# Kernel tuning notes

Hardware: AMD Instinct MI355X
Metric: run time of the kernel (lower is better)

Reference implementation:

```python
import jax, jax.numpy as jnp
import numpy as np

B, T, OBS, ENC, H, A = 32, 512, 256, 1024, 1024, 64
AR_COEF, TAR_COEF = 0.01, 0.01
LN_EPS = 1e-5


def setup_inputs() -> dict:
    key = jax.random.key(0)
    ks = jax.random.split(key, 8)
    s = 0.02  # weight scale to keep activations in a sane range
    # PyTorch LSTM bias init in source: zeros, forget-gate slice [H:2H] = 1.0 (both b_ih and b_hh)
    b_gate = jnp.zeros((4 * H,), jnp.float32).at[H:2 * H].set(1.0)
    return {
        "obs": jax.random.normal(ks[0], (B, T, OBS), jnp.float32),
        "hxs": jnp.zeros((B, H), jnp.float32),
        "cxs": jnp.zeros((B, H), jnp.float32),
        "W1": jax.random.normal(ks[1], (ENC, OBS), jnp.float32) * s,
        "b1": jnp.zeros((ENC,), jnp.float32),
        "W2": jax.random.normal(ks[2], (ENC, ENC), jnp.float32) * s,
        "b2": jnp.zeros((ENC,), jnp.float32),
        "W_ih": jax.random.normal(ks[3], (4 * H, ENC), jnp.float32) * s,
        "W_hh": jax.random.normal(ks[4], (4 * H, H), jnp.float32) * s,
        "b_ih": b_gate,
        "b_hh": b_gate,
        "ln_g": jnp.ones((H,), jnp.float32),
        "ln_b": jnp.zeros((H,), jnp.float32),
        "Wa": jax.random.normal(ks[5], (A, H), jnp.float32) * s,
        "ba": jnp.zeros((A,), jnp.float32),
        "Wc": jax.random.normal(ks[6], (1, H), jnp.float32) * s,
        "bc": jnp.zeros((1,), jnp.float32),
    }


def reference(obs, hxs, cxs, W1, b1, W2, b2, W_ih, W_hh, b_ih, b_hh,
              ln_g, ln_b, Wa, ba, Wc, bc):
    # Encoder: Linear -> SiLU -> Linear -> SiLU
    enc = jax.nn.silu(obs @ W1.T + b1)
    enc = jax.nn.silu(enc @ W2.T + b2)  # (B,T,ENC)

    # LSTM (WeightDrop is identity in eval mode / p=0). Precompute input gates.
    gx = enc @ W_ih.T + (b_ih + b_hh)  # (B,T,4H)

    def step(carry, g_t):
        h, c = carry
        g = g_t + h @ W_hh.T  # (B,4H), PyTorch gate order: i, f, g, o
        i, f, gc, o = jnp.split(g, 4, axis=-1)
        c = jax.nn.sigmoid(f) * c + jax.nn.sigmoid(i) * jnp.tanh(gc)
        h = jax.nn.sigmoid(o) * jnp.tanh(c)
        return (h, c), h

    (h_n, c_n), hs = jax.lax.scan(step, (hxs, cxs), jnp.swapaxes(gx, 0, 1))
    out = jnp.swapaxes(hs, 0, 1)  # (B,T,H)

    # LayerNorm
    mu = out.mean(-1, keepdims=True)
    var = out.var(-1, keepdims=True)
    out = (out - mu) / jnp.sqrt(var + LN_EPS) * ln_g + ln_b

    ar_loss = jnp.mean(out ** 2) * AR_COEF
    tar_loss = jnp.mean((out[:, 1:, :] - out[:, :-1, :]) ** 2) * TAR_COEF

    logits = out @ Wa.T + ba          # (B,T,A)
    values = (out @ Wc.T + bc)[..., 0]  # (B,T)
    return logits, values, h_n, c_n, ar_loss, tar_loss
```

## Files before the change

### kernel.cpp

```cpp
#include <hip/hip_runtime.h>


typedef _Float16 half8 __attribute__((ext_vector_type(8)));
typedef _Float16 half4v __attribute__((ext_vector_type(4)));
typedef float floatx4 __attribute__((ext_vector_type(4)));

__device__ __forceinline__ float sigmoidf_(float x) { return 1.f / (1.f + __expf(-x)); }

__global__ void k_convert(const float* __restrict__ src, _Float16* __restrict__ dst, int n4) {
  int i = blockIdx.x * blockDim.x + threadIdx.x;
  int stride = gridDim.x * blockDim.x;
  for (; i < n4; i += stride) {
    floatx4 v = *(const floatx4*)(src + (size_t)i * 4);
    half4v h;
    h[0] = (_Float16)v[0]; h[1] = (_Float16)v[1];
    h[2] = (_Float16)v[2]; h[3] = (_Float16)v[3];
    *(half4v*)(dst + (size_t)i * 4) = h;
  }
}

template<int EPI>
__global__ __launch_bounds__(256) void k_gemm(
    const _Float16* __restrict__ A, const _Float16* __restrict__ B,
    _Float16* __restrict__ C, const float* __restrict__ bias0,
    const float* __restrict__ bias1, int M, int N, int K)
{
  __shared__ _Float16 As[128 * 32];
  __shared__ _Float16 Bs[128 * 32];
  const int tid = threadIdx.x;
  const int l = tid & 63;
  const int w = tid >> 6;
  const int wr = w >> 1, wc = w & 1;
  const _Float16* Ab = A + (size_t)blockIdx.x * 128 * K;
  const _Float16* Bb = B + (size_t)blockIdx.y * 128 * K;

  floatx4 acc[4][4];
#pragma unroll
  for (int a = 0; a < 4; ++a)
#pragma unroll
    for (int b = 0; b < 4; ++b) acc[a][b] = (floatx4){0.f, 0.f, 0.f, 0.f};

  const int ci0 = tid, ci1 = tid + 256;
  const int r0 = ci0 >> 2, r1 = ci1 >> 2;
  const int q0 = (ci0 & 3) ^ ((r0 >> 2) & 3);
  const int q1 = (ci1 & 3) ^ ((r1 >> 2) & 3);
  const int lr = l & 15;
  const int ko = l >> 4;
  const int nkt = K >> 5;

  for (int kt = 0; kt < nkt; ++kt) {
    const _Float16* Ak = Ab + kt * 32;
    const _Float16* Bk = Bb + kt * 32;
    uint4 va0 = *(const uint4*)(Ak + (size_t)r0 * K + q0 * 8);
    uint4 va1 = *(const uint4*)(Ak + (size_t)r1 * K + q1 * 8);
    uint4 vb0 = *(const uint4*)(Bk + (size_t)r0 * K + q0 * 8);
    uint4 vb1 = *(const uint4*)(Bk + (size_t)r1 * K + q1 * 8);
    __syncthreads();
    *(uint4*)(As + ci0 * 8) = va0;
    *(uint4*)(As + ci1 * 8) = va1;
    *(uint4*)(Bs + ci0 * 8) = vb0;
    *(uint4*)(Bs + ci1 * 8) = vb1;
    __syncthreads();
    half8 af[4], bf[4];
#pragma unroll
    for (int mr = 0; mr < 4; ++mr) {
      int row = wr * 64 + mr * 16 + lr;
      int cq = ko ^ ((row >> 2) & 3);
      af[mr] = *(const half8*)(As + row * 32 + cq * 8);
    }
#pragma unroll
    for (int nc = 0; nc < 4; ++nc) {
      int col = wc * 64 + nc * 16 + lr;
      int cq = ko ^ ((col >> 2) & 3);
      bf[nc] = *(const half8*)(Bs + col * 32 + cq * 8);
    }
#pragma unroll
    for (int mr = 0; mr < 4; ++mr)
#pragma unroll
      for (int nc = 0; nc < 4; ++nc)
        acc[mr][nc] = __builtin_amdgcn_mfma_f32_16x16x32_f16(af[mr], bf[nc], acc[mr][nc], 0, 0, 0);
  }

  const int lq = l >> 4;
#pragma unroll
  for (int nc = 0; nc < 4; ++nc) {
    int gcol = blockIdx.y * 128 + wc * 64 + nc * 16 + lr;
    float bia = bias0[gcol];
    if (EPI == 1) bia += bias1[gcol];
#pragma unroll
    for (int mr = 0; mr < 4; ++mr) {
      int grow = blockIdx.x * 128 + wr * 64 + mr * 16 + lq * 4;
#pragma unroll
      for (int i = 0; i < 4; ++i) {
        float v = acc[mr][nc][i] + bia;
        if (EPI == 0) v = v * sigmoidf_(v);
        C[(size_t)(grow + i) * N + gcol] = (_Float16)v;
      }
    }
  }
}

__global__ __launch_bounds__(256, 1) void k_scan(
    const _Float16* __restrict__ gx,
    const _Float16* __restrict__ Whh,
    const float* __restrict__ cxs,
    _Float16* __restrict__ hstate,
    _Float16* __restrict__ outh,
    float* __restrict__ out_hn, float* __restrict__ out_cn,
    int* __restrict__ flags)
{
  const int blk = blockIdx.x;
  const int hbase = blk * 16;
  const int tid = threadIdx.x, l = tid & 63, w = tid >> 6;
  __shared__ float red[4][4][2][64][4];

  const int cc = l & 15, ko = l >> 4;

  half8 bfr[4][8];
#pragma unroll
  for (int q = 0; q < 4; ++q)
#pragma unroll
    for (int kk = 0; kk < 8; ++kk)
      bfr[q][kk] = *(const half8*)(Whh + (size_t)(q * 1024 + hbase + cc) * 1024
                                   + w * 256 + kk * 32 + ko * 8);

  const int gb = tid >> 3;
  const int gc2 = tid & 7;
  float c0 = cxs[gb * 1024 + hbase + gc2 * 2 + 0];
  float c1 = cxs[gb * 1024 + hbase + gc2 * 2 + 1];
  const int rg = gb >> 4, reg = gb & 3;
  const int lane0 = ((gb & 15) >> 2) * 16 + gc2 * 2;

  for (int t = 0; t < 512; ++t) {
    unsigned gxv[4];
#pragma unroll
    for (int q = 0; q < 4; ++q)
      gxv[q] = *(const unsigned*)(gx + ((size_t)gb * 512 + t) * 4096
                                  + q * 1024 + hbase + gc2 * 2);

    if (t > 0) {
      int guard = 0;
      while (true) {
        int f = __hip_atomic_load(flags + l * 16, __ATOMIC_RELAXED,
                                  __HIP_MEMORY_SCOPE_AGENT);
        if (__all(f >= t)) break;
        if (++guard > (1 << 17)) break;
        __builtin_amdgcn_s_sleep(1);
      }
      asm volatile("" ::: "memory");
    }

    const _Float16* hcur = hstate + (size_t)(t & 1) * 32768;

    unsigned long long a0lo[8], a0hi[8], a1lo[8], a1hi[8];
    {
      const unsigned long long* p0 =
          (const unsigned long long*)(hcur + cc * 1024 + w * 256 + ko * 8);
      const unsigned long long* p1 =
          (const unsigned long long*)(hcur + (16 + cc) * 1024 + w * 256 + ko * 8);
#pragma unroll
      for (int kk = 0; kk < 8; ++kk) {
        a0lo[kk] = __hip_atomic_load(p0 + kk * 8, __ATOMIC_RELAXED, __HIP_MEMORY_SCOPE_AGENT);
        a0hi[kk] = __hip_atomic_load(p0 + kk * 8 + 1, __ATOMIC_RELAXED, __HIP_MEMORY_SCOPE_AGENT);
        a1lo[kk] = __hip_atomic_load(p1 + kk * 8, __ATOMIC_RELAXED, __HIP_MEMORY_SCOPE_AGENT);
        a1hi[kk] = __hip_atomic_load(p1 + kk * 8 + 1, __ATOMIC_RELAXED, __HIP_MEMORY_SCOPE_AGENT);
      }
    }

    floatx4 acc[4][2];
#pragma unroll
    for (int q = 0; q < 4; ++q) {
      acc[q][0] = (floatx4){0.f, 0.f, 0.f, 0.f};
      acc[q][1] = (floatx4){0.f, 0.f, 0.f, 0.f};
    }
#pragma unroll
    for (int kk = 0; kk < 8; ++kk) {
      union { unsigned long long u[2]; half8 h; } ua0, ua1;
      ua0.u[0] = a0lo[kk]; ua0.u[1] = a0hi[kk];
      ua1.u[0] = a1lo[kk]; ua1.u[1] = a1hi[kk];
#pragma unroll
      for (int q = 0; q < 4; ++q) {
        acc[q][0] = __builtin_amdgcn_mfma_f32_16x16x32_f16(ua0.h, bfr[q][kk], acc[q][0], 0, 0, 0);
        acc[q][1] = __builtin_amdgcn_mfma_f32_16x16x32_f16(ua1.h, bfr[q][kk], acc[q][1], 0, 0, 0);
      }
    }
#pragma unroll
    for (int q = 0; q < 4; ++q) {
      *(floatx4*)(&red[w][q][0][l][0]) = acc[q][0];
      *(floatx4*)(&red[w][q][1][l][0]) = acc[q][1];
    }
    __syncthreads();

    float pre0[4], pre1[4];
#pragma unroll
    for (int q = 0; q < 4; ++q) {
      pre0[q] = red[0][q][rg][lane0][reg] + red[1][q][rg][lane0][reg]
              + red[2][q][rg][lane0][reg] + red[3][q][rg][lane0][reg];
      pre1[q] = red[0][q][rg][lane0 + 1][reg] + red[1][q][rg][lane0 + 1][reg]
              + red[2][q][rg][lane0 + 1][reg] + red[3][q][rg][lane0 + 1][reg];
    }
    union { unsigned u; _Float16 h[2]; } g0, g1, g2, g3;
    g0.u = gxv[0]; g1.u = gxv[1]; g2.u = gxv[2]; g3.u = gxv[3];

    float i0 = sigmoidf_(pre0[0] + (float)g0.h[0]);
    float f0 = sigmoidf_(pre0[1] + (float)g1.h[0]);
    float gg0 = tanhf(pre0[2] + (float)g2.h[0]);
    float o0 = sigmoidf_(pre0[3] + (float)g3.h[0]);
    c0 = f0 * c0 + i0 * gg0;
    float h0 = o0 * tanhf(c0);

    float i1 = sigmoidf_(pre1[0] + (float)g0.h[1]);
    float f1 = sigmoidf_(pre1[1] + (float)g1.h[1]);
    float gg1 = tanhf(pre1[2] + (float)g2.h[1]);
    float o1 = sigmoidf_(pre1[3] + (float)g3.h[1]);
    c1 = f1 * c1 + i1 * gg1;
    float h1 = o1 * tanhf(c1);

    union { _Float16 h[2]; unsigned u; } hp;
    hp.h[0] = (_Float16)h0; hp.h[1] = (_Float16)h1;

    _Float16* hnext = hstate + (size_t)((t + 1) & 1) * 32768;
    __hip_atomic_store((unsigned*)(hnext + gb * 1024 + hbase + gc2 * 2), hp.u,
                       __ATOMIC_RELAXED, __HIP_MEMORY_SCOPE_AGENT);
    *(unsigned*)(outh + ((size_t)gb * 512 + t) * 1024 + hbase + gc2 * 2) = hp.u;
    if (t == 511) {
      float2 hv; hv.x = h0; hv.y = h1;
      float2 cv; cv.x = c0; cv.y = c1;
      *(float2*)(out_hn + gb * 1024 + hbase + gc2 * 2) = hv;
      *(float2*)(out_cn + gb * 1024 + hbase + gc2 * 2) = cv;
    }

    asm volatile("s_waitcnt vmcnt(0)" ::: "memory");
    __syncthreads();
    if (tid == 0)
      __hip_atomic_store(flags + blk * 16, t + 1, __ATOMIC_RELAXED,
                         __HIP_MEMORY_SCOPE_AGENT);
  }
}

__global__ __launch_bounds__(256) void k_ln(
    const _Float16* __restrict__ x, const float* __restrict__ gam,
    const float* __restrict__ bet, _Float16* __restrict__ y,
    float* __restrict__ arpart)
{
  const int m = blockIdx.x;
  const int tid = threadIdx.x;
  const int w = tid >> 6, l = tid & 63;
  half4v v = *(const half4v*)(x + (size_t)m * 1024 + tid * 4);
  float xv[4]; float s = 0.f, ss = 0.f;
#pragma unroll
  for (int j = 0; j < 4; ++j) { xv[j] = (float)v[j]; s += xv[j]; ss += xv[j] * xv[j]; }
#pragma unroll
  for (int off = 32; off > 0; off >>= 1) { s += __shfl_xor(s, off, 64); ss += __shfl_xor(ss, off, 64); }
  __shared__ float sw[4], ssw[4], bcast[2];
  if (l == 0) { sw[w] = s; ssw[w] = ss; }
  __syncthreads();
  if (tid == 0) {
    float S = sw[0] + sw[1] + sw[2] + sw[3];
    float SS = ssw[0] + ssw[1] + ssw[2] + ssw[3];
    float mu = S * (1.f / 1024.f);
    float var = SS * (1.f / 1024.f) - mu * mu;
    bcast[0] = mu; bcast[1] = rsqrtf(var + 1e-5f);
  }
  __syncthreads();
  float mu = bcast[0], rstd = bcast[1];
  float part = 0.f; half4v o;
#pragma unroll
  for (int j = 0; j < 4; ++j) {
    float nv = (xv[j] - mu) * rstd * gam[tid * 4 + j] + bet[tid * 4 + j];
    o[j] = (_Float16)nv;
    part += nv * nv;
  }
  *(half4v*)(y + (size_t)m * 1024 + tid * 4) = o;
#pragma unroll
  for (int off = 32; off > 0; off >>= 1) part += __shfl_xor(part, off, 64);
  if (l == 0) sw[w] = part;
  __syncthreads();
  if (tid == 0) arpart[m] = sw[0] + sw[1] + sw[2] + sw[3];
}

__global__ __launch_bounds__(256) void k_tar(const _Float16* __restrict__ y, float* __restrict__ tarpart) {
  const int tid = threadIdx.x;
  int gid = blockIdx.x * 256 + tid;
  const int stride = gridDim.x * 256;
  const int TOT = 32 * 511 * 256;
  float s = 0.f;
  for (int v = gid; v < TOT; v += stride) {
    int b = v / (511 * 256);
    int r = v - b * (511 * 256);
    size_t base = (size_t)b * 512 * 1024 + (size_t)r * 4;
    half4v a = *(const half4v*)(y + base);
    half4v c = *(const half4v*)(y + base + 1024);
#pragma unroll
    for (int j = 0; j < 4; ++j) { float d = (float)c[j] - (float)a[j]; s += d * d; }
  }
#pragma unroll
  for (int off = 32; off > 0; off >>= 1) s += __shfl_xor(s, off, 64);
  __shared__ float sw[4];
  if ((tid & 63) == 0) sw[tid >> 6] = s;
  __syncthreads();
  if (tid == 0) tarpart[blockIdx.x] = sw[0] + sw[1] + sw[2] + sw[3];
}

__global__ __launch_bounds__(256) void k_reduce(
    const float* __restrict__ arpart, const float* __restrict__ tarpart,
    float* __restrict__ dst)
{
  const int tid = threadIdx.x;
  float a = 0.f, t = 0.f;
  for (int i = tid; i < 16384; i += 256) a += arpart[i];
  for (int i = tid; i < 2048; i += 256) t += tarpart[i];
#pragma unroll
  for (int off = 32; off > 0; off >>= 1) { a += __shfl_xor(a, off, 64); t += __shfl_xor(t, off, 64); }
  __shared__ float sa[4], st[4];
  if ((tid & 63) == 0) { sa[tid >> 6] = a; st[tid >> 6] = t; }
  __syncthreads();
  if (tid == 0) {
    dst[0] = (sa[0] + sa[1] + sa[2] + sa[3]) * (0.01f / 16777216.f);
    dst[1] = (st[0] + st[1] + st[2] + st[3]) * (0.01f / 16744448.f);
  }
}

__global__ __launch_bounds__(256) void k_logits(
    const _Float16* __restrict__ X, const _Float16* __restrict__ Wa,
    const float* __restrict__ ba, float* __restrict__ out)
{
  const int tid = threadIdx.x, l = tid & 63, w = tid >> 6;
  const int lr = l & 15, lq = l >> 4;
  const int rowb = blockIdx.x * 64 + w * 16;
  floatx4 acc[4];
#pragma unroll
  for (int nc = 0; nc < 4; ++nc) acc[nc] = (floatx4){0.f, 0.f, 0.f, 0.f};
  for (int kc = 0; kc < 32; ++kc) {
    int k = kc * 32 + lq * 8;
    half8 af = *(const half8*)(X + (size_t)(rowb + lr) * 1024 + k);
#pragma unroll
    for (int nc = 0; nc < 4; ++nc) {
      half8 bf = *(const half8*)(Wa + (size_t)(nc * 16 + lr) * 1024 + k);
      acc[nc] = __builtin_amdgcn_mfma_f32_16x16x32_f16(af, bf, acc[nc], 0, 0, 0);
    }
  }
#pragma unroll
  for (int nc = 0; nc < 4; ++nc) {
    int col = nc * 16 + lr;
    float bia = ba[col];
#pragma unroll
    for (int i = 0; i < 4; ++i) {
      int grow = rowb + lq * 4 + i;
      out[(size_t)grow * 64 + col] = acc[nc][i] + bia;
    }
  }
}

__global__ __launch_bounds__(256) void k_values(
    const _Float16* __restrict__ X, const _Float16* __restrict__ Wc,
    const float* __restrict__ bc, float* __restrict__ out)
{
  const int tid = threadIdx.x, l = tid & 63, w = tid >> 6;
  half8 w0 = *(const half8*)(Wc + l * 16);
  half8 w1 = *(const half8*)(Wc + l * 16 + 8);
  float bias = bc[0];
  const int rowb = blockIdx.x * 64 + w * 16;
  for (int r = 0; r < 16; ++r) {
    const _Float16* xr = X + (size_t)(rowb + r) * 1024 + l * 16;
    half8 x0 = *(const half8*)(xr);
    half8 x1 = *(const half8*)(xr + 8);
    float s = 0.f;
#pragma unroll
    for (int j = 0; j < 8; ++j) s += (float)x0[j] * (float)w0[j] + (float)x1[j] * (float)w1[j];
#pragma unroll
    for (int off = 32; off > 0; off >>= 1) s += __shfl_xor(s, off, 64);
    if (l == 0) out[rowb + r] = s + bias;
  }
}

extern "C" void kernel_launch(void* const* d_in, const int* in_sizes, int n_in,
                              void* d_out, int out_size, void* d_ws, size_t ws_size,
                              hipStream_t stream)
{
  const float* obs = (const float*)d_in[0];
  const float* hxs = (const float*)d_in[1];
  const float* cxs = (const float*)d_in[2];
  const float* W1  = (const float*)d_in[3];
  const float* b1  = (const float*)d_in[4];
  const float* W2  = (const float*)d_in[5];
  const float* b2  = (const float*)d_in[6];
  const float* Wih = (const float*)d_in[7];
  const float* Whh = (const float*)d_in[8];
  const float* bih = (const float*)d_in[9];
  const float* bhh = (const float*)d_in[10];
  const float* lng = (const float*)d_in[11];
  const float* lnb = (const float*)d_in[12];
  const float* Wa  = (const float*)d_in[13];
  const float* ba  = (const float*)d_in[14];
  const float* Wc  = (const float*)d_in[15];
  const float* bc  = (const float*)d_in[16];

  char* ws = (char*)d_ws;
  size_t off = 0;
  auto alloc = [&](size_t bytes) -> char* {
    char* p = ws + off;
    off += (bytes + 255) & ~(size_t)255;
    return p;
  };
  _Float16* obs16 = (_Float16*)alloc(4194304ull * 2);
  _Float16* W1x   = (_Float16*)alloc(262144ull * 2);
  _Float16* W2x   = (_Float16*)alloc(1048576ull * 2);
  _Float16* Wihx  = (_Float16*)alloc(4194304ull * 2);
  _Float16* Whhx  = (_Float16*)alloc(4194304ull * 2);
  _Float16* Wax   = (_Float16*)alloc(65536ull * 2);
  _Float16* Wcx   = (_Float16*)alloc(1024ull * 2);
  _Float16* enc1  = (_Float16*)alloc(16384ull * 1024 * 2);
  _Float16* enc2  = (_Float16*)alloc(16384ull * 1024 * 2);
  _Float16* gx    = (_Float16*)alloc(16384ull * 4096 * 2);
  _Float16* hstate= (_Float16*)alloc(2ull * 32 * 1024 * 2);
  _Float16* outh  = (_Float16*)alloc(16384ull * 1024 * 2);
  float* arpart   = (float*)alloc(16384ull * 4);
  float* tarpart  = (float*)alloc(2048ull * 4);
  int* flags      = (int*)alloc(64ull * 16 * 4);
  _Float16* normed = enc1;

  float* out_f      = (float*)d_out;
  float* out_logits = out_f;
  float* out_values = out_f + 1048576;
  float* out_hn     = out_f + 1064960;
  float* out_cn     = out_f + 1097728;
  float* out_loss   = out_f + 1130496;

  hipMemsetAsync(flags, 0, 64 * 16 * 4, stream);

  auto conv = [&](const float* s, _Float16* d, int n) {
    int n4 = n >> 2;
    int grid = (n4 + 255) / 256;
    if (grid > 2048) grid = 2048;
    k_convert<<<grid, 256, 0, stream>>>(s, d, n4);
  };
  conv(obs, obs16, 4194304);
  conv(W1, W1x, 262144);
  conv(W2, W2x, 1048576);
  conv(Wih, Wihx, 4194304);
  conv(Whh, Whhx, 4194304);
  conv(Wa, Wax, 65536);
  conv(Wc, Wcx, 1024);
  conv(hxs, hstate, 32768);

  k_gemm<0><<<dim3(128, 8), 256, 0, stream>>>(obs16, W1x, enc1, b1, nullptr, 16384, 1024, 256);
  k_gemm<0><<<dim3(128, 8), 256, 0, stream>>>(enc1, W2x, enc2, b2, nullptr, 16384, 1024, 1024);
  k_gemm<1><<<dim3(128, 32), 256, 0, stream>>>(enc2, Wihx, gx, bih, bhh, 16384, 4096, 1024);
  k_scan<<<64, 256, 0, stream>>>(gx, Whhx, cxs, hstate, outh, out_hn, out_cn, flags);
  k_ln<<<16384, 256, 0, stream>>>(outh, lng, lnb, normed, arpart);
  k_tar<<<2048, 256, 0, stream>>>(normed, tarpart);
  k_reduce<<<1, 256, 0, stream>>>(arpart, tarpart, out_loss);
  k_logits<<<256, 256, 0, stream>>>(normed, Wax, ba, out_logits);
  k_values<<<256, 256, 0, stream>>>(normed, Wcx, bc, out_values);
  (void)in_sizes; (void)n_in; (void)out_size; (void)ws_size;
}
```

Measured before the change: 3.453 ms.

## Replace per-block flag barrier with step-tagged hidden-state words in LSTM scan

The recurrent scan no longer publishes a per-block flag after a waitcnt and barrier. Each fp16 pair of the hidden state is now stored in a 64-bit word whose upper half holds the step number. Consumers spin directly on the data they need until every tag is current, so the flag round trip and the store-drain wait are gone. This doubles the hidden-state traffic and makes every wave poll 64 atomic loads per retry. The reduction scratch array is also padded to cut LDS bank conflicts.

```diff
diff --git a/kernel.cpp b/kernel.cpp
--- a/kernel.cpp
+++ b/kernel.cpp
@@ -4,6 +4,7 @@
 typedef _Float16 half8 __attribute__((ext_vector_type(8)));
 typedef _Float16 half4v __attribute__((ext_vector_type(4)));
 typedef float floatx4 __attribute__((ext_vector_type(4)));
+typedef unsigned long long ull;
 
 __device__ __forceinline__ float sigmoidf_(float x) { return 1.f / (1.f + __expf(-x)); }
 
@@ -17,6 +18,16 @@
     h[2] = (_Float16)v[2]; h[3] = (_Float16)v[3];
     *(half4v*)(dst + (size_t)i * 4) = h;
   }
+}
+
+__global__ __launch_bounds__(256) void k_inith(const float* __restrict__ hxs,
+                                               ull* __restrict__ hT) {
+  int s = blockIdx.x * 256 + threadIdx.x;
+  int batch = s >> 9, pair = s & 511;
+  union { _Float16 h[2]; unsigned u; } p;
+  p.h[0] = (_Float16)hxs[batch * 1024 + pair * 2];
+  p.h[1] = (_Float16)hxs[batch * 1024 + pair * 2 + 1];
+  hT[s] = (ull)p.u | (1ull << 32);
 }
 
 template<int EPI>
@@ -104,15 +115,14 @@
     const _Float16* __restrict__ gx,
     const _Float16* __restrict__ Whh,
     const float* __restrict__ cxs,
-    _Float16* __restrict__ hstate,
+    ull* __restrict__ hT,
     _Float16* __restrict__ outh,
-    float* __restrict__ out_hn, float* __restrict__ out_cn,
-    int* __restrict__ flags)
+    float* __restrict__ out_hn, float* __restrict__ out_cn)
 {
   const int blk = blockIdx.x;
   const int hbase = blk * 16;
-  const int tid = threadIdx.x, l = tid & 63, w = tid >> 6;
-  __shared__ float red[4][4][2][64][4];
+  const int tid = threadIdx.x, l = tid & 63, wq = tid >> 6;
+  __shared__ float red[4][4][2][4][65];
 
   const int cc = l & 15, ko = l >> 4;
 
@@ -122,13 +132,12 @@
 #pragma unroll
     for (int kk = 0; kk < 8; ++kk)
       bfr[q][kk] = *(const half8*)(Whh + (size_t)(q * 1024 + hbase + cc) * 1024
-                                   + w * 256 + kk * 32 + ko * 8);
-
-  const int gb = tid >> 3;
-  const int gc2 = tid & 7;
+                                   + wq * 256 + kk * 32 + ko * 8);
+
+  const int gb = tid >> 3, gc2 = tid & 7;
   float c0 = cxs[gb * 1024 + hbase + gc2 * 2 + 0];
   float c1 = cxs[gb * 1024 + hbase + gc2 * 2 + 1];
-  const int rg = gb >> 4, reg = gb & 3;
+  const int gmt = gb >> 4, greg = gb & 3;
   const int lane0 = ((gb & 15) >> 2) * 16 + gc2 * 2;
 
   for (int t = 0; t < 512; ++t) {
@@ -138,33 +147,26 @@
       gxv[q] = *(const unsigned*)(gx + ((size_t)gb * 512 + t) * 4096
                                   + q * 1024 + hbase + gc2 * 2);
 
-    if (t > 0) {
-      int guard = 0;
-      while (true) {
-        int f = __hip_atomic_load(flags + l * 16, __ATOMIC_RELAXED,
-                                  __HIP_MEMORY_SCOPE_AGENT);
-        if (__all(f >= t)) break;
-        if (++guard > (1 << 17)) break;
-        __builtin_amdgcn_s_sleep(1);
-      }
-      asm volatile("" ::: "memory");
-    }
-
-    const _Float16* hcur = hstate + (size_t)(t & 1) * 32768;
-
-    unsigned long long a0lo[8], a0hi[8], a1lo[8], a1hi[8];
-    {
-      const unsigned long long* p0 =
-          (const unsigned long long*)(hcur + cc * 1024 + w * 256 + ko * 8);
-      const unsigned long long* p1 =
-          (const unsigned long long*)(hcur + (16 + cc) * 1024 + w * 256 + ko * 8);
-#pragma unroll
-      for (int kk = 0; kk < 8; ++kk) {
-        a0lo[kk] = __hip_atomic_load(p0 + kk * 8, __ATOMIC_RELAXED, __HIP_MEMORY_SCOPE_AGENT);
-        a0hi[kk] = __hip_atomic_load(p0 + kk * 8 + 1, __ATOMIC_RELAXED, __HIP_MEMORY_SCOPE_AGENT);
-        a1lo[kk] = __hip_atomic_load(p1 + kk * 8, __ATOMIC_RELAXED, __HIP_MEMORY_SCOPE_AGENT);
-        a1hi[kk] = __hip_atomic_load(p1 + kk * 8 + 1, __ATOMIC_RELAXED, __HIP_MEMORY_SCOPE_AGENT);
-      }
+    const ull* base0 = hT + (size_t)(t & 1) * 16384 + (size_t)cc * 512;
+    const ull* base1 = base0 + 16 * 512;
+    const unsigned tgt = (unsigned)(t + 1);
+    ull ld0[32], ld1[32];
+    int guard = 0;
+    while (true) {
+      bool ok = true;
+#pragma unroll
+      for (int kk = 0; kk < 8; ++kk)
+#pragma unroll
+        for (int j = 0; j < 4; ++j) {
+          int p = wq * 128 + kk * 16 + ko * 4 + j;
+          ld0[kk * 4 + j] = __hip_atomic_load(base0 + p, __ATOMIC_RELAXED, __HIP_MEMORY_SCOPE_AGENT);
+          ld1[kk * 4 + j] = __hip_atomic_load(base1 + p, __ATOMIC_RELAXED, __HIP_MEMORY_SCOPE_AGENT);
+        }
+#pragma unroll
+      for (int i = 0; i < 32; ++i)
+        ok &= ((unsigned)(ld0[i] >> 32) >= tgt) & ((unsigned)(ld1[i] >> 32) >= tgt);
+      if (__all(ok)) break;
+      if (++guard > (1 << 15)) break;
     }
 
     floatx4 acc[4][2];
@@ -175,29 +177,34 @@
     }
 #pragma unroll
     for (int kk = 0; kk < 8; ++kk) {
-      union { unsigned long long u[2]; half8 h; } ua0, ua1;
-      ua0.u[0] = a0lo[kk]; ua0.u[1] = a0hi[kk];
-      ua1.u[0] = a1lo[kk]; ua1.u[1] = a1hi[kk];
+      union { unsigned u[4]; half8 h; } a0, a1;
+#pragma unroll
+      for (int j = 0; j < 4; ++j) {
+        a0.u[j] = (unsigned)ld0[kk * 4 + j];
+        a1.u[j] = (unsigned)ld1[kk * 4 + j];
+      }
 #pragma unroll
       for (int q = 0; q < 4; ++q) {
-        acc[q][0] = __builtin_amdgcn_mfma_f32_16x16x32_f16(ua0.h, bfr[q][kk], acc[q][0], 0, 0, 0);
-        acc[q][1] = __builtin_amdgcn_mfma_f32_16x16x32_f16(ua1.h, bfr[q][kk], acc[q][1], 0, 0, 0);
+        acc[q][0] = __builtin_amdgcn_mfma_f32_16x16x32_f16(a0.h, bfr[q][kk], acc[q][0], 0, 0, 0);
+        acc[q][1] = __builtin_amdgcn_mfma_f32_16x16x32_f16(a1.h, bfr[q][kk], acc[q][1], 0, 0, 0);
       }
     }
 #pragma unroll
+    for (int q = 0; q < 4; ++q)
+#pragma unroll
+      for (int mt = 0; mt < 2; ++mt)
+#pragma unroll
+        for (int i = 0; i < 4; ++i)
+          red[wq][q][mt][i][l] = acc[q][mt][i];
+    __syncthreads();
+
+    float pre0[4], pre1[4];
+#pragma unroll
     for (int q = 0; q < 4; ++q) {
-      *(floatx4*)(&red[w][q][0][l][0]) = acc[q][0];
-      *(floatx4*)(&red[w][q][1][l][0]) = acc[q][1];
-    }
-    __syncthreads();
-
-    float pre0[4], pre1[4];
-#pragma unroll
-    for (int q = 0; q < 4; ++q) {
-      pre0[q] = red[0][q][rg][lane0][reg] + red[1][q][rg][lane0][reg]
-              + red[2][q][rg][lane0][reg] + red[3][q][rg][lane0][reg];
-      pre1[q] = red[0][q][rg][lane0 + 1][reg] + red[1][q][rg][lane0 + 1][reg]
-              + red[2][q][rg][lane0 + 1][reg] + red[3][q][rg][lane0 + 1][reg];
+      pre0[q] = red[0][q][gmt][greg][lane0] + red[1][q][gmt][greg][lane0]
+              + red[2][q][gmt][greg][lane0] + red[3][q][gmt][greg][lane0];
+      pre1[q] = red[0][q][gmt][greg][lane0 + 1] + red[1][q][gmt][greg][lane0 + 1]
+              + red[2][q][gmt][greg][lane0 + 1] + red[3][q][gmt][greg][lane0 + 1];
     }
     union { unsigned u; _Float16 h[2]; } g0, g1, g2, g3;
     g0.u = gxv[0]; g1.u = gxv[1]; g2.u = gxv[2]; g3.u = gxv[3];
@@ -219,9 +226,9 @@
     union { _Float16 h[2]; unsigned u; } hp;
     hp.h[0] = (_Float16)h0; hp.h[1] = (_Float16)h1;
 
-    _Float16* hnext = hstate + (size_t)((t + 1) & 1) * 32768;
-    __hip_atomic_store((unsigned*)(hnext + gb * 1024 + hbase + gc2 * 2), hp.u,
-                       __ATOMIC_RELAXED, __HIP_MEMORY_SCOPE_AGENT);
+    ull st = (ull)hp.u | ((ull)(unsigned)(t + 2) << 32);
+    __hip_atomic_store(hT + (size_t)((t + 1) & 1) * 16384 + gb * 512 + blk * 8 + gc2,
+                       st, __ATOMIC_RELAXED, __HIP_MEMORY_SCOPE_AGENT);
     *(unsigned*)(outh + ((size_t)gb * 512 + t) * 1024 + hbase + gc2 * 2) = hp.u;
     if (t == 511) {
       float2 hv; hv.x = h0; hv.y = h1;
@@ -229,12 +236,7 @@
       *(float2*)(out_hn + gb * 1024 + hbase + gc2 * 2) = hv;
       *(float2*)(out_cn + gb * 1024 + hbase + gc2 * 2) = cv;
     }
-
-    asm volatile("s_waitcnt vmcnt(0)" ::: "memory");
     __syncthreads();
-    if (tid == 0)
-      __hip_atomic_store(flags + blk * 16, t + 1, __ATOMIC_RELAXED,
-                         __HIP_MEMORY_SCOPE_AGENT);
   }
 }
 
@@ -413,11 +415,10 @@
   _Float16* enc1  = (_Float16*)alloc(16384ull * 1024 * 2);
   _Float16* enc2  = (_Float16*)alloc(16384ull * 1024 * 2);
   _Float16* gx    = (_Float16*)alloc(16384ull * 4096 * 2);
-  _Float16* hstate= (_Float16*)alloc(2ull * 32 * 1024 * 2);
+  ull* hT         = (ull*)alloc(2ull * 16384 * 8);
   _Float16* outh  = (_Float16*)alloc(16384ull * 1024 * 2);
   float* arpart   = (float*)alloc(16384ull * 4);
   float* tarpart  = (float*)alloc(2048ull * 4);
-  int* flags      = (int*)alloc(64ull * 16 * 4);
   _Float16* normed = enc1;
 
   float* out_f      = (float*)d_out;
@@ -427,7 +428,8 @@
   float* out_cn     = out_f + 1097728;
   float* out_loss   = out_f + 1130496;
 
-  hipMemsetAsync(flags, 0, 64 * 16 * 4, stream);
+  hipMemsetAsync(hT, 0, 2ull * 16384 * 8, stream);
+  k_inith<<<64, 256, 0, stream>>>(hxs, hT);
 
   auto conv = [&](const float* s, _Float16* d, int n) {
     int n4 = n >> 2;
@@ -442,12 +444,11 @@
   conv(Whh, Whhx, 4194304);
   conv(Wa, Wax, 65536);
   conv(Wc, Wcx, 1024);
-  conv(hxs, hstate, 32768);
 
   k_gemm<0><<<dim3(128, 8), 256, 0, stream>>>(obs16, W1x, enc1, b1, nullptr, 16384, 1024, 256);
   k_gemm<0><<<dim3(128, 8), 256, 0, stream>>>(enc1, W2x, enc2, b2, nullptr, 16384, 1024, 1024);
   k_gemm<1><<<dim3(128, 32), 256, 0, stream>>>(enc2, Wihx, gx, bih, bhh, 16384, 4096, 1024);
-  k_scan<<<64, 256, 0, stream>>>(gx, Whhx, cxs, hstate, outh, out_hn, out_cn, flags);
+  k_scan<<<64, 256, 0, stream>>>(gx, Whhx, cxs, hT, outh, out_hn, out_cn);
   k_ln<<<16384, 256, 0, stream>>>(outh, lng, lnb, normed, arpart);
   k_tar<<<2048, 256, 0, stream>>>(normed, tarpart);
   k_reduce<<<1, 256, 0, stream>>>(arpart, tarpart, out_loss);
```

Measured after the change: 6.879 ms. 99.2% more time.
